# Kernel tuning notes

Hardware: AMD Instinct MI355X
Metric: run time of the kernel (lower is better)

Reference implementation:

```python
import jax, jax.numpy as jnp
import numpy as np

D_MODEL = 4096
D_FF = 11008
M = 8192
GROUP = 128
NLEVELS = 16  # 4-bit


def setup_inputs() -> dict:
    key = jax.random.key(0)
    ks = jax.random.split(key, 10)
    def qw(k, K, N):
        return jax.random.randint(k, (K, N), 0, NLEVELS, dtype=jnp.int32)
    def qz(k, G, N):
        return jax.random.randint(k, (G, N), 0, NLEVELS, dtype=jnp.int32)
    def sc(k, G, N):
        # small positive per-group scales, roughly matching real AWQ magnitudes
        return jax.random.uniform(k, (G, N), dtype=jnp.float32) * 0.02 + 1e-3
    return {
        "x": jax.random.normal(ks[0], (M, D_MODEL), dtype=jnp.float32),
        "q_gate": qw(ks[1], D_MODEL, D_FF),
        "z_gate": qz(ks[2], D_MODEL // GROUP, D_FF),
        "s_gate": sc(ks[3], D_MODEL // GROUP, D_FF),
        "q_up": qw(ks[4], D_MODEL, D_FF),
        "z_up": qz(ks[5], D_MODEL // GROUP, D_FF),
        "s_up": sc(ks[6], D_MODEL // GROUP, D_FF),
        "q_down": qw(ks[7], D_FF, D_MODEL),
        "z_down": qz(ks[8], D_FF // GROUP, D_MODEL),
        "s_down": sc(ks[9], D_FF // GROUP, D_MODEL),
        "group_size": GROUP,
    }


def _dequant(q, z, s, group_size):
    # q: [K, N] int4 values; z: [K//G, N] zeros; s: [K//G, N] scales
    K, N = q.shape
    G = group_size
    w = (q.astype(s.dtype).reshape(K // G, G, N) - z.astype(s.dtype)[:, None, :]) * s[:, None, :]
    return w.reshape(K, N)


def reference(x, q_gate, z_gate, s_gate, q_up, z_up, s_up, q_down, z_down, s_down, group_size):
    gate = x @ _dequant(q_gate, z_gate, s_gate, group_size)   # [M, D_FF]
    up = x @ _dequant(q_up, z_up, s_up, group_size)           # [M, D_FF]
    h = jax.nn.silu(gate) * up                                # SwiGLU
    return h @ _dequant(q_down, z_down, s_down, group_size)   # [M, D_MODEL]
```

## Files before the change

### kernel.cpp

```cpp
#include <hip/hip_runtime.h>
#include <cstdint>

typedef unsigned short u16;
typedef unsigned int u32;
typedef unsigned char u8;
typedef signed char s8;
typedef __bf16 bf16_t;
typedef bf16_t bf16x8 __attribute__((ext_vector_type(8)));
typedef float f32x4 __attribute__((ext_vector_type(4)));
typedef int i32x4 __attribute__((ext_vector_type(4)));

#define DMODEL 4096
#define DFF 11008
#define MROWS 8192

__device__ __forceinline__ u16 f2bf(float f) {
  u32 u = __builtin_bit_cast(u32, f);
  u += 0x7FFFu + ((u >> 16) & 1u);
  return (u16)(u >> 16);
}
__device__ __forceinline__ float bf2f(u16 h) {
  return __builtin_bit_cast(float, (u32)h << 16);
}

#define GLD16(gptr, lptr)                                                  \
  __builtin_amdgcn_global_load_lds(                                        \
      (const __attribute__((address_space(1))) u32*)(gptr),                \
      (__attribute__((address_space(3))) u32*)(lptr), 16, 0, 0)

#define BAR asm volatile("s_barrier" ::: "memory")
#define VM4 asm volatile("s_waitcnt vmcnt(4)" ::: "memory")
#define LGKM0 asm volatile("s_waitcnt lgkmcnt(0)" ::: "memory")

__global__ void k_quant_x(const float* __restrict__ x, s8* __restrict__ x8,
                          float* __restrict__ sx) {
  const int row = blockIdx.x;
  const int t = threadIdx.x;
  const int lane = t & 63, wid = t >> 6;
  const float4* xr = reinterpret_cast<const float4*>(x + (size_t)row * DMODEL);
  float4 v[4];
  float m = 0.f;
#pragma unroll
  for (int i = 0; i < 4; ++i) {
    v[i] = xr[t * 4 + i];
    m = fmaxf(m, fmaxf(fmaxf(fabsf(v[i].x), fabsf(v[i].y)),
                       fmaxf(fabsf(v[i].z), fabsf(v[i].w))));
  }
#pragma unroll
  for (int off = 32; off >= 1; off >>= 1) m = fmaxf(m, __shfl_xor(m, off));
  __shared__ float wm[4];
  if (lane == 0) wm[wid] = m;
  __syncthreads();
  float mall = fmaxf(fmaxf(wm[0], wm[1]), fmaxf(wm[2], wm[3]));
  mall = fmaxf(mall, 1e-8f);
  const float inv = 127.f / mall;
  if (t == 0) sx[row] = mall / 127.f;
  uint4 o;
  u32 p[4];
#pragma unroll
  for (int i = 0; i < 4; ++i) {
    int a = (int)rintf(v[i].x * inv), b = (int)rintf(v[i].y * inv);
    int c = (int)rintf(v[i].z * inv), d = (int)rintf(v[i].w * inv);
    p[i] = (u32)(a & 255) | ((u32)(b & 255) << 8) | ((u32)(c & 255) << 16) |
           ((u32)(d & 255) << 24);
  }
  o.x = p[0]; o.y = p[1]; o.z = p[2]; o.w = p[3];
  reinterpret_cast<uint4*>(x8 + (size_t)row * DMODEL)[t] = o;
}

__global__ void k_dequant_T8(const int* __restrict__ q, const int* __restrict__ z,
                             s8* __restrict__ w8, int K, int N) {
  __shared__ s8 tile[32][40];
  const int t = threadIdx.x;
  const int n0 = blockIdx.x << 5, k0 = blockIdx.y << 5;
  {
    const int kr = t >> 3, n4 = (t & 7) << 2;
    const int k = k0 + kr, g = k >> 7;
    const int4 qv = *reinterpret_cast<const int4*>(&q[(size_t)k * N + n0 + n4]);
    const int4 zv = *reinterpret_cast<const int4*>(&z[(size_t)g * N + n0 + n4]);
    tile[kr][n4 + 0] = (s8)(qv.x - zv.x);
    tile[kr][n4 + 1] = (s8)(qv.y - zv.y);
    tile[kr][n4 + 2] = (s8)(qv.z - zv.z);
    tile[kr][n4 + 3] = (s8)(qv.w - zv.w);
  }
  __syncthreads();
  {
    const int n = t >> 3, ks = (t & 7) << 2;
    uchar4 o;
    o.x = (u8)tile[ks + 0][n];
    o.y = (u8)tile[ks + 1][n];
    o.z = (u8)tile[ks + 2][n];
    o.w = (u8)tile[ks + 3][n];
    *reinterpret_cast<uchar4*>(&w8[(size_t)(n0 + n) * K + k0 + ks]) = o;
  }
}

__global__ void k_dequant_T(const int* __restrict__ q, const int* __restrict__ z,
                            const float* __restrict__ s, u16* __restrict__ wT,
                            int K, int N) {
  __shared__ u16 tile[32][36];
  const int t = threadIdx.x;
  const int n0 = blockIdx.x << 5, k0 = blockIdx.y << 5;
  {
    const int kr = t >> 3, n4 = (t & 7) << 2;
    const int k = k0 + kr, g = k >> 7;
    const int4 qv = *reinterpret_cast<const int4*>(&q[(size_t)k * N + n0 + n4]);
    const int4 zv = *reinterpret_cast<const int4*>(&z[(size_t)g * N + n0 + n4]);
    const float4 sv = *reinterpret_cast<const float4*>(&s[(size_t)g * N + n0 + n4]);
    ushort4 o;
    o.x = f2bf((float)(qv.x - zv.x) * sv.x);
    o.y = f2bf((float)(qv.y - zv.y) * sv.y);
    o.z = f2bf((float)(qv.z - zv.z) * sv.z);
    o.w = f2bf((float)(qv.w - zv.w) * sv.w);
    *reinterpret_cast<ushort4*>(&tile[kr][n4]) = o;
  }
  __syncthreads();
  {
    const int n = t >> 3, ks = (t & 7) << 2;
    ushort4 o;
    o.x = tile[ks + 0][n];
    o.y = tile[ks + 1][n];
    o.z = tile[ks + 2][n];
    o.w = tile[ks + 3][n];
    *reinterpret_cast<ushort4*>(&wT[(size_t)(n0 + n) * K + k0 + ks]) = o;
  }
}

__global__ __launch_bounds__(512, 2) void k_fused_i8(
    const s8* __restrict__ A, const s8* __restrict__ Bg,
    const s8* __restrict__ Bu, const float* __restrict__ sx,
    const float* __restrict__ sg, const float* __restrict__ su,
    u16* __restrict__ H) {
  constexpr int Kdim = DMODEL;
  constexpr int ntiles = Kdim >> 6;
  __shared__ s8 Ab[3][256 * 64];
  __shared__ s8 Bgb[3][128 * 64];
  __shared__ s8 Bub[3][128 * 64];
  __shared__ float scl[2][32 * 128];

  const int midx = blockIdx.x & 31, nidx = blockIdx.x >> 5;
  const int m0 = midx << 8, n0 = nidx << 7;
  const int t = threadIdx.x;
  const int lane = t & 63;
  const int wid = t >> 6;
  const int wr = wid >> 2, wc = wid & 3;
  const int r16 = lane & 15, quad = lane >> 4;

  const int lrow = lane >> 2;
  const int sswz = ((lane & 3) ^ ((lrow >> 1) & 3)) << 4;
  const s8* Asrc = A + (size_t)(m0 + wid * 16 + lrow) * Kdim + sswz;
  const s8* Gsrc = Bg + (size_t)(n0 + wid * 16 + lrow) * Kdim + sswz;
  const s8* Usrc = Bu + (size_t)(n0 + wid * 16 + lrow) * Kdim + sswz;
  const size_t rstepA = (size_t)128 * Kdim;
  const int ldst = wid * 1024;

#define STG(tt, bs) do {                                                   \
    size_t ko = (size_t)((tt) & (ntiles - 1)) << 6;                        \
    GLD16(Asrc + ko,          &Ab[bs][ldst]);                              \
    GLD16(Asrc + ko + rstepA, &Ab[bs][ldst + 8192]);                       \
    GLD16(Gsrc + ko,          &Bgb[bs][ldst]);                             \
    GLD16(Usrc + ko,          &Bub[bs][ldst]);                             \
  } while (0)

  const int aswz = (quad ^ ((r16 >> 1) & 3)) << 4;
  const int abase = (wr * 128 + r16) * 64 + aswz;
  const int bbase = (wc * 32 + r16) * 64 + aswz;

  f32x4 facg[8][2], facu[8][2];
  const f32x4 zf = {0.f, 0.f, 0.f, 0.f};
#pragma unroll
  for (int mf = 0; mf < 8; ++mf)
#pragma unroll
    for (int nf = 0; nf < 2; ++nf) { facg[mf][nf] = zf; facu[mf][nf] = zf; }
  const i32x4 zi = {0, 0, 0, 0};

#pragma unroll
  for (int k = 0; k < 2; ++k) {
    int j = t + k * 512;
    int g = j >> 5;
    int c = (j & 31) << 2;
    *reinterpret_cast<float4*>(&scl[0][g * 128 + c]) =
        *reinterpret_cast<const float4*>(&sg[(size_t)g * DFF + n0 + c]);
    *reinterpret_cast<float4*>(&scl[1][g * 128 + c]) =
        *reinterpret_cast<const float4*>(&su[(size_t)g * DFF + n0 + c]);
  }
  STG(0, 0); STG(1, 1);
  VM4;
  LGKM0;
  BAR;

  const int sloc = wc * 32 + r16;

  int cur = 0, nb = 2;
  for (int p = 0; p < ntiles; ++p) {
    i32x4 av[8], bgv[2], buv[2];
#pragma unroll
    for (int mf = 0; mf < 8; ++mf)
      av[mf] = *reinterpret_cast<const i32x4*>(&Ab[cur][abase + mf * 1024]);
#pragma unroll
    for (int nf = 0; nf < 2; ++nf) {
      bgv[nf] = *reinterpret_cast<const i32x4*>(&Bgb[cur][bbase + nf * 1024]);
      buv[nf] = *reinterpret_cast<const i32x4*>(&Bub[cur][bbase + nf * 1024]);
    }
    const int g = p >> 1;
    float s_g0 = scl[0][g * 128 + sloc];
    float s_g1 = scl[0][g * 128 + sloc + 16];
    float s_u0 = scl[1][g * 128 + sloc];
    float s_u1 = scl[1][g * 128 + sloc + 16];
    STG(p + 2, nb);
    VM4;
    __builtin_amdgcn_s_setprio(1);
#pragma unroll
    for (int mf = 0; mf < 8; ++mf) {
      i32x4 ig0 = __builtin_amdgcn_mfma_i32_16x16x64_i8(av[mf], bgv[0], zi, 0, 0, 0);
      i32x4 ig1 = __builtin_amdgcn_mfma_i32_16x16x64_i8(av[mf], bgv[1], zi, 0, 0, 0);
      i32x4 iu0 = __builtin_amdgcn_mfma_i32_16x16x64_i8(av[mf], buv[0], zi, 0, 0, 0);
      i32x4 iu1 = __builtin_amdgcn_mfma_i32_16x16x64_i8(av[mf], buv[1], zi, 0, 0, 0);
#pragma unroll
      for (int j = 0; j < 4; ++j) {
        facg[mf][0][j] += (float)ig0[j] * s_g0;
        facg[mf][1][j] += (float)ig1[j] * s_g1;
        facu[mf][0][j] += (float)iu0[j] * s_u0;
        facu[mf][1][j] += (float)iu1[j] * s_u1;
      }
    }
    __builtin_amdgcn_s_setprio(0);
    BAR;
    cur = (cur == 2) ? 0 : cur + 1;
    nb = (nb == 2) ? 0 : nb + 1;
  }
  asm volatile("s_waitcnt vmcnt(0)" ::: "memory");

  const int rb0 = m0 + wr * 128 + quad * 4;
  const int cb0 = n0 + wc * 32 + r16;
#pragma unroll
  for (int mf = 0; mf < 8; ++mf) {
#pragma unroll
    for (int j = 0; j < 4; ++j) {
      const int row = rb0 + mf * 16 + j;
      const float sxr = sx[row];
#pragma unroll
      for (int nf = 0; nf < 2; ++nf) {
        float gv = facg[mf][nf][j] * sxr;
        float uv = facu[mf][nf][j] * sxr;
        float sv = gv / (1.f + __expf(-gv));
        H[(size_t)row * DFF + cb0 + nf * 16] = f2bf(sv * uv);
      }
    }
  }
#undef STG
}

__global__ __launch_bounds__(512, 2) void k_down(
    const u16* __restrict__ A, const u16* __restrict__ BT,
    float* __restrict__ C) {
  constexpr int Ndim = DMODEL, Kdim = DFF;
  __shared__ u16 As[2][2][256 * 32];
  __shared__ u16 Bs[2][2][256 * 32];

  const int nidx = blockIdx.x & 15;
  const int midx = blockIdx.x >> 4;
  const int m0 = midx << 8;
  const int n0 = nidx << 8;
  const int t = threadIdx.x;
  const int lane = t & 63;
  const int wid = t >> 6;
  const int wr = wid >> 2, wc = wid & 3;
  const int r16 = lane & 15, quad = lane >> 4;

  const int lrow4 = lane >> 2;
  const int sslot = ((lane & 3) ^ ((lane >> 3) & 3)) << 3;
  const u16* Asrc = A + (size_t)(m0 + wid * 16 + lrow4) * Kdim + sslot;
  const u16* Bsrc = BT + (size_t)(n0 + wid * 16 + lrow4) * Kdim + sslot;
  const size_t rstep = (size_t)128 * Kdim;
  const int lbo = wid * 512;
  constexpr int ntiles = Kdim >> 6;

#define SA(tt, kh, bf) do {                                                \
    int ttw = (tt) < ntiles ? (tt) : (tt) - ntiles;                        \
    size_t ko = ((size_t)ttw << 6) + ((kh) << 5);                          \
    GLD16(Asrc + ko,         &As[bf][kh][lbo]);                            \
    GLD16(Asrc + ko + rstep, &As[bf][kh][lbo + 4096]);                     \
  } while (0)
#define SB(tt, kh, bf) do {                                                \
    int ttw = (tt) < ntiles ? (tt) : (tt) - ntiles;                        \
    size_t ko = ((size_t)ttw << 6) + ((kh) << 5);                          \
    GLD16(Bsrc + ko,         &Bs[bf][kh][lbo]);                            \
    GLD16(Bsrc + ko + rstep, &Bs[bf][kh][lbo + 4096]);                     \
  } while (0)

  const int fragoff = (quad ^ ((r16 >> 1) & 3)) << 3;
  const int abase = (wr * 128 + r16) * 32 + fragoff;
  const int bbase = (wc * 64 + r16) * 32 + fragoff;

  f32x4 acc[8][4];
  const f32x4 zf = {0.f, 0.f, 0.f, 0.f};
#pragma unroll
  for (int mf = 0; mf < 8; ++mf)
#pragma unroll
    for (int nf = 0; nf < 4; ++nf) acc[mf][nf] = zf;

  bf16x8 avA[4], av2A[4], bvA[4];
  bf16x8 avB[4], av2B[4], bvB[4];

#define PFD(av_, av2_, bv_, bf, kk) do {                                   \
    _Pragma("unroll") for (int ii = 0; ii < 4; ++ii) {                     \
      av_[ii] = *reinterpret_cast<const bf16x8*>(                          \
          &As[bf][kk][abase + ii * 512]);                                  \
      av2_[ii] = *reinterpret_cast<const bf16x8*>(                         \
          &As[bf][kk][abase + 2048 + ii * 512]);                           \
    }                                                                      \
    _Pragma("unroll") for (int nn = 0; nn < 4; ++nn)                       \
      bv_[nn] = *reinterpret_cast<const bf16x8*>(                          \
          &Bs[bf][kk][bbase + nn * 512]);                                  \
  } while (0)

#define PHD(av_, av2_, bv_, nav_, nav2_, nbv_, STG_, VMW, bfn, kkn) do {   \
    STG_;                                                                  \
    VMW;                                                                   \
    BAR;                                                                   \
    __builtin_amdgcn_s_setprio(1);                                         \
    _Pragma("unroll") for (int ii = 0; ii < 4; ++ii)                       \
      _Pragma("unroll") for (int nn = 0; nn < 4; ++nn)                     \
        acc[ii][nn] = __builtin_amdgcn_mfma_f32_16x16x32_bf16(             \
            av_[ii], bv_[nn], acc[ii][nn], 0, 0, 0);                       \
    PFD(nav_, nav2_, nbv_, bfn, kkn);                                      \
    _Pragma("unroll") for (int ii = 0; ii < 4; ++ii)                       \
      _Pragma("unroll") for (int nn = 0; nn < 4; ++nn)                     \
        acc[4 + ii][nn] = __builtin_amdgcn_mfma_f32_16x16x32_bf16(         \
            av2_[ii], bv_[nn], acc[4 + ii][nn], 0, 0, 0);                  \
    __builtin_amdgcn_s_setprio(0);                                         \
    BAR;                                                                   \
  } while (0)

  SA(0, 0, 0); SB(0, 0, 0); SA(0, 1, 0); SB(0, 1, 0); SA(1, 0, 1); SB(1, 0, 1);
  VM4;
  BAR;
  PFD(avA, av2A, bvA, 0, 0);

  constexpr int NI = ntiles >> 1;
  for (int it = 0; it < NI; ++it) {
    const int t0 = it * 2;
    PHD(avA, av2A, bvA, avB, av2B, bvB,
        { SA(t0 + 1, 1, 1); SB(t0 + 1, 1, 1); }, (void)0, 0, 1);
    PHD(avB, av2B, bvB, avA, av2A, bvA,
        { SA(t0 + 2, 0, 0); SB(t0 + 2, 0, 0); }, VM4, 1, 0);
    PHD(avA, av2A, bvA, avB, av2B, bvB,
        { SA(t0 + 2, 1, 0); SB(t0 + 2, 1, 0); }, (void)0, 1, 1);
    PHD(avB, av2B, bvB, avA, av2A, bvA,
        { SA(t0 + 3, 0, 1); SB(t0 + 3, 0, 1); }, VM4, 0, 0);
  }
  asm volatile("s_waitcnt vmcnt(0)" ::: "memory");

  const int rb0 = m0 + wr * 128 + quad * 4;
  const int cb0 = n0 + wc * 64 + r16;
#pragma unroll
  for (int mf = 0; mf < 8; ++mf) {
#pragma unroll
    for (int nf = 0; nf < 4; ++nf) {
      f32x4 v = acc[mf][nf];
      int row = rb0 + mf * 16;
      int col = cb0 + nf * 16;
#pragma unroll
      for (int j = 0; j < 4; ++j)
        C[(size_t)(row + j) * Ndim + col] = v[j];
    }
  }
#undef SA
#undef SB
#undef PFD
#undef PHD
}

extern "C" void kernel_launch(void* const* d_in, const int* in_sizes, int n_in,
                              void* d_out, int out_size, void* d_ws, size_t ws_size,
                              hipStream_t stream) {
  const float* x  = (const float*)d_in[0];
  const int*   qg = (const int*)d_in[1];
  const int*   zg = (const int*)d_in[2];
  const float* sg = (const float*)d_in[3];
  const int*   qu = (const int*)d_in[4];
  const int*   zu = (const int*)d_in[5];
  const float* su = (const float*)d_in[6];
  const int*   qd = (const int*)d_in[7];
  const int*   zd = (const int*)d_in[8];
  const float* sd = (const float*)d_in[9];
  float* out = (float*)d_out;

  char* ws = (char*)d_ws;
  const size_t szX8 = (size_t)MROWS * DMODEL;
  const size_t szSX = (size_t)MROWS * 4;
  const size_t szW8 = (size_t)DMODEL * DFF;
  const size_t szWD = (size_t)DFF * DMODEL * 2;
  s8*    x8  = (s8*)(ws);
  float* sx  = (float*)(ws + szX8);
  s8*    wg8 = (s8*)(ws + szX8 + szSX);
  s8*    wu8 = (s8*)(ws + szX8 + szSX + szW8);
  u16*   wdT = (u16*)(ws + szX8 + szSX + 2 * szW8);
  u16*   h   = (u16*)(ws + szX8 + szSX + 2 * szW8 + szWD);

  k_quant_x<<<MROWS, 256, 0, stream>>>(x, x8, sx);
  k_dequant_T8<<<dim3(DFF / 32, DMODEL / 32), 256, 0, stream>>>(qg, zg, wg8, DMODEL, DFF);
  k_dequant_T8<<<dim3(DFF / 32, DMODEL / 32), 256, 0, stream>>>(qu, zu, wu8, DMODEL, DFF);
  k_dequant_T<<<dim3(DMODEL / 32, DFF / 32), 256, 0, stream>>>(qd, zd, sd, wdT, DFF, DMODEL);

  k_fused_i8<<<(MROWS / 256) * (DFF / 128), 512, 0, stream>>>(
      x8, wg8, wu8, sx, sg, su, h);
  k_down<<<(MROWS / 256) * (DMODEL / 256), 512, 0, stream>>>(h, wdT, out);
}
```

Before: 2.051 ms.

## Process two K-tiles per iteration, accumulating int MFMA before one scale step

The gate/up kernel's main loop now handles the two K-tiles of each scale group together. The int32 MFMA results of both tiles are chained in the accumulator, so the int-to-float convert and scale FMA run once per group rather than once per tile. The triple-buffer schedule is reworked: two stage loads are issued per iteration around a mid-iteration barrier, and each iteration ends with a full vmcnt(0) wait. This halves the epilogue-style float work and barrier count per tile, but the full wait per iteration may expose global-load latency that the previous vmcnt(4) pipeline hid.

```diff
diff --git a/kernel.cpp b/kernel.cpp
--- a/kernel.cpp
+++ b/kernel.cpp
@@ -29,6 +29,7 @@
       (__attribute__((address_space(3))) u32*)(lptr), 16, 0, 0)
 
 #define BAR asm volatile("s_barrier" ::: "memory")
+#define VM0 asm volatile("s_waitcnt vmcnt(0)" ::: "memory")
 #define VM4 asm volatile("s_waitcnt vmcnt(4)" ::: "memory")
 #define LGKM0 asm volatile("s_waitcnt lgkmcnt(0)" ::: "memory")
 
@@ -185,37 +186,48 @@
         *reinterpret_cast<const float4*>(&su[(size_t)g * DFF + n0 + c]);
   }
   STG(0, 0); STG(1, 1);
-  VM4;
+  VM0;
   LGKM0;
   BAR;
 
   const int sloc = wc * 32 + r16;
 
-  int cur = 0, nb = 2;
-  for (int p = 0; p < ntiles; ++p) {
-    i32x4 av[8], bgv[2], buv[2];
+  int cur = 0;
+  for (int i = 0; i < (ntiles >> 1); ++i) {
+    const int a = cur;
+    const int b = (a + 1 < 3) ? a + 1 : a - 2;
+    const int c = (a + 2 < 3) ? a + 2 : a - 1;
+    i32x4 av0[8], bg_a[2], bg_b[2], bu_a[2], bu_b[2];
 #pragma unroll
     for (int mf = 0; mf < 8; ++mf)
-      av[mf] = *reinterpret_cast<const i32x4*>(&Ab[cur][abase + mf * 1024]);
+      av0[mf] = *reinterpret_cast<const i32x4*>(&Ab[a][abase + mf * 1024]);
 #pragma unroll
     for (int nf = 0; nf < 2; ++nf) {
-      bgv[nf] = *reinterpret_cast<const i32x4*>(&Bgb[cur][bbase + nf * 1024]);
-      buv[nf] = *reinterpret_cast<const i32x4*>(&Bub[cur][bbase + nf * 1024]);
+      bg_a[nf] = *reinterpret_cast<const i32x4*>(&Bgb[a][bbase + nf * 1024]);
+      bu_a[nf] = *reinterpret_cast<const i32x4*>(&Bub[a][bbase + nf * 1024]);
+      bg_b[nf] = *reinterpret_cast<const i32x4*>(&Bgb[b][bbase + nf * 1024]);
+      bu_b[nf] = *reinterpret_cast<const i32x4*>(&Bub[b][bbase + nf * 1024]);
     }
-    const int g = p >> 1;
-    float s_g0 = scl[0][g * 128 + sloc];
-    float s_g1 = scl[0][g * 128 + sloc + 16];
-    float s_u0 = scl[1][g * 128 + sloc];
-    float s_u1 = scl[1][g * 128 + sloc + 16];
-    STG(p + 2, nb);
-    VM4;
+    float s_g0 = scl[0][i * 128 + sloc];
+    float s_g1 = scl[0][i * 128 + sloc + 16];
+    float s_u0 = scl[1][i * 128 + sloc];
+    float s_u1 = scl[1][i * 128 + sloc + 16];
+    STG(2 * i + 2, c);
+    LGKM0;
+    BAR;
+    STG(2 * i + 3, a);
     __builtin_amdgcn_s_setprio(1);
 #pragma unroll
     for (int mf = 0; mf < 8; ++mf) {
-      i32x4 ig0 = __builtin_amdgcn_mfma_i32_16x16x64_i8(av[mf], bgv[0], zi, 0, 0, 0);
-      i32x4 ig1 = __builtin_amdgcn_mfma_i32_16x16x64_i8(av[mf], bgv[1], zi, 0, 0, 0);
-      i32x4 iu0 = __builtin_amdgcn_mfma_i32_16x16x64_i8(av[mf], buv[0], zi, 0, 0, 0);
-      i32x4 iu1 = __builtin_amdgcn_mfma_i32_16x16x64_i8(av[mf], buv[1], zi, 0, 0, 0);
+      i32x4 a1 = *reinterpret_cast<const i32x4*>(&Ab[b][abase + mf * 1024]);
+      i32x4 ig0 = __builtin_amdgcn_mfma_i32_16x16x64_i8(av0[mf], bg_a[0], zi, 0, 0, 0);
+      i32x4 ig1 = __builtin_amdgcn_mfma_i32_16x16x64_i8(av0[mf], bg_a[1], zi, 0, 0, 0);
+      i32x4 iu0 = __builtin_amdgcn_mfma_i32_16x16x64_i8(av0[mf], bu_a[0], zi, 0, 0, 0);
+      i32x4 iu1 = __builtin_amdgcn_mfma_i32_16x16x64_i8(av0[mf], bu_a[1], zi, 0, 0, 0);
+      ig0 = __builtin_amdgcn_mfma_i32_16x16x64_i8(a1, bg_b[0], ig0, 0, 0, 0);
+      ig1 = __builtin_amdgcn_mfma_i32_16x16x64_i8(a1, bg_b[1], ig1, 0, 0, 0);
+      iu0 = __builtin_amdgcn_mfma_i32_16x16x64_i8(a1, bu_b[0], iu0, 0, 0, 0);
+      iu1 = __builtin_amdgcn_mfma_i32_16x16x64_i8(a1, bu_b[1], iu1, 0, 0, 0);
 #pragma unroll
       for (int j = 0; j < 4; ++j) {
         facg[mf][0][j] += (float)ig0[j] * s_g0;
@@ -225,11 +237,10 @@
       }
     }
     __builtin_amdgcn_s_setprio(0);
+    VM0;
     BAR;
-    cur = (cur == 2) ? 0 : cur + 1;
-    nb = (nb == 2) ? 0 : nb + 1;
-  }
-  asm volatile("s_waitcnt vmcnt(0)" ::: "memory");
+    cur = c;
+  }
 
   const int rb0 = m0 + wr * 128 + quad * 4;
   const int cb0 = n0 + wc * 32 + r16;
```

Measured after the change: 2.163 ms. 5.4% more time.
